# Optimization experiments

Hardware: AMD Instinct MI355X
Metric: run time of the kernel (lower is better)

The kernel has to match this reference:

```python
import jax, jax.numpy as jnp
import numpy as np
import math

MAX_DELAY = 25
TAU = 2.0
VTH = 1.0
BN_EPS = 1e-5
ATAN_ALPHA = 2.0


def build_dcls_kernel(W, P, SIG, D):
    # Gaussian-interpolated DCLS kernel ('gauss' version).
    # W, P, SIG: (O, I, K) -> kernel (O, I, D)
    lim = D // 2
    j = jnp.arange(D, dtype=W.dtype)                      # (D,)
    Pc = jnp.clip(P, -lim, lim) + lim                     # (O, I, K)
    sig = jnp.abs(SIG) + 0.27
    g = jnp.exp(-0.5 * ((j - Pc[..., None]) / sig[..., None]) ** 2)  # (O,I,K,D)
    g = g / (g.sum(-1, keepdims=True) + 1e-7)
    return jnp.einsum('oik,oikd->oid', W, g)


def dcls_conv_positive(x, W, P, SIG, D):
    # Dale-positive: abs(weight) before kernel construction; padding=0 (VALID)
    k = build_dcls_kernel(jnp.abs(W), P, SIG, D)
    return jax.lax.conv_general_dilated(
        x, k, window_strides=(1,), padding='VALID',
        dimension_numbers=('NCW', 'OIW', 'NCW'))


def batchnorm_m(x, gamma, beta):
    # spikingjelly layer.BatchNorm1d step_mode='m' on (T, B, C):
    # flattens (T*B) as batch, normalizes per channel (training-mode stats).
    mean = x.mean(axis=(0, 1))
    var = x.var(axis=(0, 1))
    return (x - mean) * jax.lax.rsqrt(var + BN_EPS) * gamma + beta


def lif_multistep(x_seq, tau, v_th):
    # LIFNode, decay_input=False, v_reset=0 (hard reset), detach_reset=True,
    # ATan surrogate. x_seq: (T, B, C).
    inv_tau = jnp.asarray(1.0 / tau, x_seq.dtype)
    def step(v, xt):
        v = v * (1.0 - inv_tau) + xt              # charge (decay_input=False)
        u = v - v_th
        sg = jnp.arctan(0.5 * math.pi * ATAN_ALPHA * u) / math.pi + 0.5
        hard = (u >= 0).astype(xt.dtype)
        spike = sg + jax.lax.stop_gradient(hard - sg)
        v = v * (1.0 - jax.lax.stop_gradient(spike))   # hard reset, detached
        return v, spike
    v0 = jnp.zeros(x_seq.shape[1:], x_seq.dtype)
    _, spikes = jax.lax.scan(step, v0, x_seq)
    return spikes


def setup_inputs() -> dict:
    key = jax.random.key(0)
    ks = jax.random.split(key, 8)
    B, C_in, T = 64, 700, 300
    n_out, n_inh, K = 256, 128, 1
    return {
        'x': jax.random.normal(ks[0], (B, C_in, T), jnp.float32),
        'W_inh': jax.random.normal(ks[1], (n_inh, C_in, K), jnp.float32),
        'P_inh': jax.random.normal(ks[2], (n_inh, C_in, K), jnp.float32),
        'SIG_inh': jax.random.uniform(ks[3], (n_inh, C_in, K), jnp.float32),
        'W_exc': jax.random.normal(ks[4], (n_out, C_in, K), jnp.float32),
        'P_exc': jax.random.normal(ks[5], (n_out, C_in, K), jnp.float32),
        'SIG_exc': jax.random.uniform(ks[6], (n_out, C_in, K), jnp.float32),
        'w_exc_inh': jax.random.uniform(ks[7], (n_out, n_inh), jnp.float32),
        'bn_gamma': jnp.ones((n_inh,), jnp.float32),
        'bn_beta': jnp.zeros((n_inh,), jnp.float32),
    }


def reference(x, W_inh, P_inh, SIG_inh, W_exc, P_exc, SIG_exc, w_exc_inh,
              bn_gamma, bn_beta):
    # inhibitory branch
    in_inhib = dcls_conv_positive(x, W_inh, P_inh, SIG_inh, MAX_DELAY)  # (B,Ci,T')
    in_inhib = jnp.transpose(in_inhib, (2, 0, 1))                       # (T',B,Ci)
    in_inhib = batchnorm_m(in_inhib, bn_gamma, bn_beta)
    spikes = lif_multistep(in_inhib, TAU, VTH)                          # (T',B,Ci)
    out_inhib = jnp.einsum('tbi,oi->tbo', spikes, -jnp.abs(w_exc_inh))
    out_inhib = jnp.transpose(out_inhib, (1, 2, 0))                     # (B,O,T')
    # excitatory branch
    excit = dcls_conv_positive(x, W_exc, P_exc, SIG_exc, MAX_DELAY)     # (B,O,T')
    return excit + out_inhib
```

## Files before the change

### kernel.cpp

```cpp
#include <hip/hip_runtime.h>
#include <math.h>

#define CI   700
#define TIN  300
#define DD   25
#define TOUT 276
#define BB   64
#define OINH 128
#define OEXC 256

#define TROWS 312
#define IPAD  704

typedef __attribute__((ext_vector_type(8))) short short8;
typedef __attribute__((ext_vector_type(4))) float f32x4;
typedef __attribute__((ext_vector_type(8))) unsigned short ushort8v;

static __device__ __forceinline__ unsigned short f2bf(float f) {
    unsigned int u = __float_as_uint(f);
    unsigned int r = (u + 0x7FFFu + ((u >> 16) & 1u)) >> 16;
    return (unsigned short)r;
}
static __device__ __forceinline__ float bf2f(unsigned short h) {
    return __uint_as_float(((unsigned int)h) << 16);
}

static __device__ __forceinline__ void gload_lds16(const void* g, void* l) {
    __builtin_amdgcn_global_load_lds(
        (const __attribute__((address_space(1))) unsigned int*)g,
        (__attribute__((address_space(3))) unsigned int*)l, 16, 0, 0);
}

__global__ void build_kt(const float* __restrict__ W, const float* __restrict__ P,
                         const float* __restrict__ SIG, float* __restrict__ kt, int O) {
    int n = blockIdx.x * 256 + threadIdx.x;
    if (n >= O * CI) return;
    int o = n % O;
    int i = n / O;
    float w   = fabsf(W[o * CI + i]);
    float p   = fminf(fmaxf(P[o * CI + i], -12.f), 12.f) + 12.f;
    float sig = fabsf(SIG[o * CI + i]) + 0.27f;
    float inv = 1.f / sig;
    float g[DD];
    float sum = 0.f;
#pragma unroll
    for (int d = 0; d < DD; ++d) {
        float e = ((float)d - p) * inv;
        g[d] = expf(-0.5f * e * e);
        sum += g[d];
    }
    float sc = w / (sum + 1e-7f);
#pragma unroll
    for (int d = 0; d < DD; ++d)
        kt[(i * DD + d) * O + o] = g[d] * sc;
}

__global__ void kexc_build(const float* __restrict__ W, const float* __restrict__ P,
                           const float* __restrict__ SIG, unsigned short* __restrict__ kb2) {
    int n = blockIdx.x * 256 + threadIdx.x;
    if (n >= OEXC * IPAD) return;
    int o = n / IPAD, ip = n % IPAD;
    if (ip >= CI) {
#pragma unroll
        for (int d = 0; d < DD; ++d)
            kb2[((size_t)d * OEXC + o) * IPAD + ip] = 0;
        return;
    }
    float w   = fabsf(W[o * CI + ip]);
    float p   = fminf(fmaxf(P[o * CI + ip], -12.f), 12.f) + 12.f;
    float sig = fabsf(SIG[o * CI + ip]) + 0.27f;
    float inv = 1.f / sig;
    float g[DD];
    float sum = 0.f;
#pragma unroll
    for (int d = 0; d < DD; ++d) {
        float e = ((float)d - p) * inv;
        g[d] = expf(-0.5f * e * e);
        sum += g[d];
    }
    float sc = w / (sum + 1e-7f);
#pragma unroll
    for (int d = 0; d < DD; ++d)
        kb2[((size_t)d * OEXC + o) * IPAD + ip] = f2bf(g[d] * sc);
}

__global__ void kinh_build(const float* __restrict__ W, const float* __restrict__ P,
                           const float* __restrict__ SIG,
                           unsigned short* __restrict__ kbh, unsigned short* __restrict__ kbl) {
    int n = blockIdx.x * 256 + threadIdx.x;
    if (n >= OINH * IPAD) return;
    int o = n / IPAD, ip = n % IPAD;
    if (ip >= CI) {
#pragma unroll
        for (int d = 0; d < DD; ++d) {
            kbh[((size_t)d * OINH + o) * IPAD + ip] = 0;
            kbl[((size_t)d * OINH + o) * IPAD + ip] = 0;
        }
        return;
    }
    float w   = fabsf(W[o * CI + ip]);
    float p   = fminf(fmaxf(P[o * CI + ip], -12.f), 12.f) + 12.f;
    float sig = fabsf(SIG[o * CI + ip]) + 0.27f;
    float inv = 1.f / sig;
    float g[DD];
    float sum = 0.f;
#pragma unroll
    for (int d = 0; d < DD; ++d) {
        float e = ((float)d - p) * inv;
        g[d] = expf(-0.5f * e * e);
        sum += g[d];
    }
    float sc = w / (sum + 1e-7f);
#pragma unroll
    for (int d = 0; d < DD; ++d) {
        float v = g[d] * sc;
        unsigned short h = f2bf(v);
        kbh[((size_t)d * OINH + o) * IPAD + ip] = h;
        kbl[((size_t)d * OINH + o) * IPAD + ip] = f2bf(v - bf2f(h));
    }
}

__global__ __launch_bounds__(256)
void xt_kernel(const float* __restrict__ x, unsigned short* __restrict__ xTh,
               unsigned short* __restrict__ xTl) {
    __shared__ float tile[64][65];
    const int tid = threadIdx.x;
    const int t0 = blockIdx.x * 64, i0 = blockIdx.y * 64, b = blockIdx.z;
#pragma unroll
    for (int s = 0; s < 16; ++s) {
        int f = s * 256 + tid;
        int tt = f & 63, ii = f >> 6;
        float v = 0.f;
        if (t0 + tt < TIN && i0 + ii < CI)
            v = x[((size_t)b * CI + i0 + ii) * TIN + t0 + tt];
        tile[tt][ii] = v;
    }
    __syncthreads();
#pragma unroll
    for (int s = 0; s < 2; ++s) {
        int f = s * 256 + tid;
        int tt = f >> 3, g = f & 7;
        if (t0 + tt < TROWS) {
            ushort8v vh, vl;
#pragma unroll
            for (int e = 0; e < 8; ++e) {
                float v = tile[tt][g * 8 + e];
                unsigned short h = f2bf(v);
                vh[e] = h;
                vl[e] = f2bf(v - bf2f(h));
            }
            size_t off = ((size_t)b * TROWS + t0 + tt) * IPAD + i0 + g * 8;
            *(ushort8v*)(xTh + off) = vh;
            if (xTl) *(ushort8v*)(xTl + off) = vl;
        }
    }
}

__global__ void wt_kernel(const float* __restrict__ w, float* __restrict__ wt) {
    int n = blockIdx.x * 256 + threadIdx.x;
    if (n >= OINH * OEXC) return;
    int o = n % OEXC, c = n / OEXC;
    wt[c * OEXC + o] = -fabsf(w[o * OINH + c]);
}

__global__ __launch_bounds__(128)
void conv_fused_v3(const unsigned short* __restrict__ xTh, const unsigned short* __restrict__ xTl,
                   const unsigned short* __restrict__ kb2,
                   const unsigned short* __restrict__ kbh, const unsigned short* __restrict__ kbl,
                   float* __restrict__ pexc0, float* __restrict__ pexc1,
                   float* __restrict__ pinh0, float* __restrict__ pinh1) {
    __shared__ unsigned short lds[20480];

    const int tid  = threadIdx.x;
    const int wave = tid >> 6;
    const int lane = tid & 63;
    const int l15 = lane & 15, l4 = lane >> 4;
    const int tt   = blockIdx.x % 3;
    const int ksp  = blockIdx.x / 3;
    const int role = blockIdx.y;
    const int b    = blockIdx.z;
    const int t0   = tt * 96;
    const int icb  = ksp * 11;

    const int ld_r = lane >> 2;
    const int ld_c = (((lane & 3) ^ ((lane >> 3) & 3)) << 4);
    const int SA   = (l15 >> 1) & 3;

    const size_t xstride = (size_t)IPAD * 2;
    const char* xh_base = (const char*)xTh + ((size_t)b * TROWS + t0) * xstride;
    const char* xl_base = (const char*)xTl + ((size_t)b * TROWS + t0) * xstride;

    if (role < 2) {
        unsigned short* xs = lds;
        unsigned short* ks = lds + 4096;
        const int o0 = role * 128 + wave * 64;

        f32x4 acc[4][6];
#pragma unroll
        for (int i = 0; i < 4; ++i)
#pragma unroll
            for (int j = 0; j < 6; ++j) acc[i][j] = (f32x4)0.f;

        for (int c = 0; c < 11; ++c) {
            const size_t cb = (size_t)(icb + c) * 64;
            __syncthreads();
            for (int j = wave; j < 8; j += 2)
                gload_lds16(xh_base + (size_t)(16 * j + ld_r) * xstride + cb + ld_c,
                            (char*)xs + j * 1024);
#pragma unroll
            for (int q = 0; q < 2; ++q) {
                const char* kbase = (const char*)kb2 + ((size_t)(q * OEXC) + o0) * xstride + cb;
                char* kdst = (char*)ks + (q * 2 + wave) * 4096;
#pragma unroll
                for (int j = 0; j < 4; ++j)
                    gload_lds16(kbase + (size_t)(16 * j + ld_r) * xstride + ld_c,
                                kdst + j * 1024);
            }
            asm volatile("s_waitcnt vmcnt(4)" ::: "memory");
            __syncthreads();

            int cur = 0;
            for (int d = 0; d < DD; ++d) {
                if (d < DD - 2) {
                    int nb = cur + 2; if (nb >= 3) nb -= 3;
                    const char* kbase = (const char*)kb2 +
                        ((size_t)((d + 2) * OEXC) + o0) * xstride + cb;
                    char* kdst = (char*)ks + (nb * 2 + wave) * 4096;
#pragma unroll
                    for (int j = 0; j < 4; ++j)
                        gload_lds16(kbase + (size_t)(16 * j + ld_r) * xstride + ld_c,
                                    kdst + j * 1024);
                }
                const char* kp = (const char*)ks + (cur * 2 + wave) * 4096;
                short8 A[4];
#pragma unroll
                for (int i = 0; i < 4; ++i)
                    A[i] = *(const short8*)(kp + (i * 16 + l15) * 64 + ((l4 ^ SA) << 4));
#pragma unroll
                for (int j = 0; j < 6; ++j) {
                    const int tr = j * 16 + l15 + d;
                    short8 Bv = *(const short8*)((const char*)xs + tr * 64 +
                                                 ((l4 ^ ((tr >> 1) & 3)) << 4));
#pragma unroll
                    for (int i = 0; i < 4; ++i)
                        acc[i][j] = __builtin_amdgcn_mfma_f32_16x16x32_bf16(
                            A[i], Bv, acc[i][j], 0, 0, 0);
                }
                if (d < DD - 2)
                    asm volatile("s_waitcnt vmcnt(4)" ::: "memory");
                else if (d == DD - 2)
                    asm volatile("s_waitcnt vmcnt(0)" ::: "memory");
                cur = (cur == 2) ? 0 : cur + 1;
            }
        }
        float* dst = ksp ? pexc1 : pexc0;
#pragma unroll
        for (int i = 0; i < 4; ++i)
#pragma unroll
            for (int j = 0; j < 6; ++j) {
                const int t = t0 + j * 16 + l15;
                if (t < TOUT) {
                    float* op = dst + ((size_t)b * OEXC + o0 + i * 16 + l4 * 4) * TOUT + t;
#pragma unroll
                    for (int r = 0; r < 4; ++r) op[(size_t)r * TOUT] = acc[i][j][r];
                }
            }
    } else {
        unsigned short* xsh = lds;
        unsigned short* xsl = lds + 4096;
        unsigned short* kws = lds + 8192;
        const int o0  = (role - 2) * 64;
        const int o0w = o0 + wave * 32;

        f32x4 acc[2][6];
#pragma unroll
        for (int i = 0; i < 2; ++i)
#pragma unroll
            for (int j = 0; j < 6; ++j) acc[i][j] = (f32x4)0.f;

        for (int c = 0; c < 11; ++c) {
            const size_t cb = (size_t)(icb + c) * 64;
            __syncthreads();
            for (int j = wave; j < 8; j += 2) {
                gload_lds16(xh_base + (size_t)(16 * j + ld_r) * xstride + cb + ld_c,
                            (char*)xsh + j * 1024);
                gload_lds16(xl_base + (size_t)(16 * j + ld_r) * xstride + cb + ld_c,
                            (char*)xsl + j * 1024);
            }
#pragma unroll
            for (int q = 0; q < 2; ++q) {
                const size_t ko = ((size_t)(q * OINH) + o0w) * xstride + cb;
                char* kdst = (char*)kws + (q * 2 + wave) * 4096;
#pragma unroll
                for (int j = 0; j < 2; ++j) {
                    gload_lds16((const char*)kbh + ko + (size_t)(16 * j + ld_r) * xstride + ld_c,
                                kdst + j * 1024);
                    gload_lds16((const char*)kbl + ko + (size_t)(16 * j + ld_r) * xstride + ld_c,
                                kdst + 2048 + j * 1024);
                }
            }
            asm volatile("s_waitcnt vmcnt(4)" ::: "memory");
            __syncthreads();

            int cur = 0;
            for (int d = 0; d < DD; ++d) {
                if (d < DD - 2) {
                    int nb = cur + 2; if (nb >= 3) nb -= 3;
                    const size_t ko = ((size_t)((d + 2) * OINH) + o0w) * xstride + cb;
                    char* kdst = (char*)kws + (nb * 2 + wave) * 4096;
#pragma unroll
                    for (int j = 0; j < 2; ++j) {
                        gload_lds16((const char*)kbh + ko + (size_t)(16 * j + ld_r) * xstride + ld_c,
                                    kdst + j * 1024);
                        gload_lds16((const char*)kbl + ko + (size_t)(16 * j + ld_r) * xstride + ld_c,
                                    kdst + 2048 + j * 1024);
                    }
                }
                const char* kp = (const char*)kws + (cur * 2 + wave) * 4096;
                short8 Ah[2], Al[2];
#pragma unroll
                for (int i = 0; i < 2; ++i) {
                    Ah[i] = *(const short8*)(kp + (i * 16 + l15) * 64 + ((l4 ^ SA) << 4));
                    Al[i] = *(const short8*)(kp + 2048 + (i * 16 + l15) * 64 + ((l4 ^ SA) << 4));
                }
#pragma unroll
                for (int j = 0; j < 6; ++j) {
                    const int tr = j * 16 + l15 + d;
                    const int xo = tr * 64 + ((l4 ^ ((tr >> 1) & 3)) << 4);
                    short8 Bh = *(const short8*)((const char*)xsh + xo);
                    short8 Bl = *(const short8*)((const char*)xsl + xo);
#pragma unroll
                    for (int i = 0; i < 2; ++i) {
                        acc[i][j] = __builtin_amdgcn_mfma_f32_16x16x32_bf16(
                            Ah[i], Bh, acc[i][j], 0, 0, 0);
                        acc[i][j] = __builtin_amdgcn_mfma_f32_16x16x32_bf16(
                            Ah[i], Bl, acc[i][j], 0, 0, 0);
                        acc[i][j] = __builtin_amdgcn_mfma_f32_16x16x32_bf16(
                            Al[i], Bh, acc[i][j], 0, 0, 0);
                    }
                }
                if (d < DD - 2)
                    asm volatile("s_waitcnt vmcnt(4)" ::: "memory");
                else if (d == DD - 2)
                    asm volatile("s_waitcnt vmcnt(0)" ::: "memory");
                cur = (cur == 2) ? 0 : cur + 1;
            }
        }
        float* dst = ksp ? pinh1 : pinh0;
#pragma unroll
        for (int i = 0; i < 2; ++i)
#pragma unroll
            for (int j = 0; j < 6; ++j) {
                const int t = t0 + j * 16 + l15;
                if (t < TOUT) {
                    float* op = dst + ((size_t)b * OINH + o0w + i * 16 + l4 * 4) * TOUT + t;
#pragma unroll
                    for (int r = 0; r < 4; ++r) op[(size_t)r * TOUT] = acc[i][j][r];
                }
            }
    }
}

__global__ void add_exc(const float* __restrict__ p1, float* __restrict__ out) {
    int n = blockIdx.x * 256 + threadIdx.x;
    float4 a = ((const float4*)out)[n];
    float4 v = ((const float4*)p1)[n];
    a.x += v.x; a.y += v.y; a.z += v.z; a.w += v.w;
    ((float4*)out)[n] = a;
}

__global__ void bn_stats2(float* __restrict__ cinh, const float* __restrict__ q1,
                          const float* __restrict__ gamma, const float* __restrict__ beta,
                          float* __restrict__ scale, float* __restrict__ shift) {
    const int c = blockIdx.x, tid = threadIdx.x;
    float sum = 0.f, sq = 0.f;
    for (int idx = tid; idx < BB * TOUT; idx += 256) {
        int b = idx / TOUT, t = idx - b * TOUT;
        size_t off = (size_t)(b * OINH + c) * TOUT + t;
        float v = cinh[off] + q1[off];
        cinh[off] = v;
        sum += v; sq += v * v;
    }
#pragma unroll
    for (int off = 32; off; off >>= 1) {
        sum += __shfl_down(sum, off);
        sq  += __shfl_down(sq, off);
    }
    __shared__ float ls[8];
    int wid = tid >> 6;
    if ((tid & 63) == 0) { ls[wid * 2] = sum; ls[wid * 2 + 1] = sq; }
    __syncthreads();
    if (tid == 0) {
        float S = 0.f, Q = 0.f;
#pragma unroll
        for (int wv = 0; wv < 4; ++wv) { S += ls[wv * 2]; Q += ls[wv * 2 + 1]; }
        const float n = (float)(BB * TOUT);
        float mean = S / n;
        float var  = Q / n - mean * mean;
        float rs   = 1.f / sqrtf(var + 1e-5f);
        float sc   = gamma[c] * rs;
        scale[c] = sc;
        shift[c] = beta[c] - mean * sc;
    }
}

__global__ __launch_bounds__(128)
void lif2(const float* __restrict__ cinh, const float* __restrict__ scale,
          const float* __restrict__ shift, unsigned char* __restrict__ spk) {
    __shared__ float tile[128 * 65];
    const int b = blockIdx.x, c = threadIdx.x;
    const float sc = scale[c], sh = shift[c];
    const float* base = cinh + (size_t)b * OINH * TOUT;
    float v = 0.f;
    for (int tc = 0; tc < TOUT; tc += 64) {
        const int len = (TOUT - tc < 64) ? (TOUT - tc) : 64;
        const int L4 = len >> 2;
        __syncthreads();
        for (int q = c; q < 128 * L4; q += 128) {
            int cc = q / L4, e = q - cc * L4;
            float4 vv = *(const float4*)(base + (size_t)cc * TOUT + tc + e * 4);
            float* dstp = &tile[cc * 65 + e * 4];
            dstp[0] = vv.x; dstp[1] = vv.y; dstp[2] = vv.z; dstp[3] = vv.w;
        }
        __syncthreads();
        for (int t2 = 0; t2 < len; ++t2) {
            float xin = tile[c * 65 + t2] * sc + sh;
            v = 0.5f * v + xin;
            bool s = (v >= 1.f);
            spk[((size_t)(tc + t2) * BB + b) * OINH + c] = s ? 1 : 0;
            v = s ? 0.f : v;
        }
    }
}

__global__ __launch_bounds__(128)
void conv_mfma(const unsigned short* __restrict__ xTh, const unsigned short* __restrict__ kb2,
               float* __restrict__ out) {
    __shared__ unsigned short xs[120 * 64];
    __shared__ unsigned short ks[2][2][64 * 64];

    const int tid  = threadIdx.x;
    const int wave = tid >> 6;
    const int lane = tid & 63;
    const int l15 = lane & 15, l4 = lane >> 4, l7 = lane & 7;
    const int b  = blockIdx.z;
    const int t0 = blockIdx.x * 96;
    const int o0 = blockIdx.y * 128 + wave * 64;

    const int ld_row = lane >> 3;
    const int ld_swz = ((l7 ^ ld_row) << 4);

    f32x4 acc[4][6];
#pragma unroll
    for (int i = 0; i < 4; ++i)
#pragma unroll
        for (int j = 0; j < 6; ++j) acc[i][j] = (f32x4)0.f;

    const char* xrow0 = (const char*)xTh + ((size_t)b * TROWS + t0) * (IPAD * 2);

    for (int ic = 0; ic < 11; ++ic) {
        const int ic0 = ic * 64;
        __syncthreads();
        for (int j = wave; j < 15; j += 2)
            gload_lds16(xrow0 + (size_t)(8 * j + ld_row) * (IPAD * 2) + ic0 * 2 + ld_swz,
                        (char*)xs + j * 1024);
        {
            const char* ksrc = (const char*)kb2 + ((size_t)o0) * (IPAD * 2) + ic0 * 2;
            char* kdst = (char*)ks + (0 * 2 + wave) * 8192;
#pragma unroll
            for (int j = 0; j < 8; ++j)
                gload_lds16(ksrc + (size_t)(8 * j + ld_row) * (IPAD * 2) + ld_swz,
                            kdst + j * 1024);
        }
        asm volatile("s_waitcnt vmcnt(0)" ::: "memory");
        __syncthreads();

        for (int d = 0; d < DD; ++d) {
            const int cur = d & 1;
            if (d < DD - 1) {
                const char* ksrc = (const char*)kb2 +
                    ((size_t)(d + 1) * OEXC + o0) * (IPAD * 2) + ic0 * 2;
                char* kdst = (char*)ks + ((cur ^ 1) * 2 + wave) * 8192;
#pragma unroll
                for (int j = 0; j < 8; ++j)
                    gload_lds16(ksrc + (size_t)(8 * j + ld_row) * (IPAD * 2) + ld_swz,
                                kdst + j * 1024);
            }
            const char* kp = (const char*)ks + (cur * 2 + wave) * 8192;
#pragma unroll
            for (int ks2 = 0; ks2 < 2; ++ks2) {
                const int cg = ks2 * 4 + l4;
                short8 A[4];
#pragma unroll
                for (int i = 0; i < 4; ++i)
                    A[i] = *(const short8*)(kp + (i * 16 + l15) * 128 + ((cg ^ l7) << 4));
#pragma unroll
                for (int j = 0; j < 6; ++j) {
                    const int tr = j * 16 + l15 + d;
                    short8 Bv = *(const short8*)((const char*)xs + tr * 128 +
                                                 ((cg ^ (tr & 7)) << 4));
#pragma unroll
                    for (int i = 0; i < 4; ++i)
                        acc[i][j] = __builtin_amdgcn_mfma_f32_16x16x32_bf16(
                            A[i], Bv, acc[i][j], 0, 0, 0);
                }
            }
            asm volatile("s_waitcnt vmcnt(0)" ::: "memory");
        }
    }

#pragma unroll
    for (int i = 0; i < 4; ++i)
#pragma unroll
        for (int j = 0; j < 6; ++j) {
            const int tt = t0 + j * 16 + l15;
            if (tt < TOUT) {
                float* op = out + ((size_t)b * OEXC + o0 + i * 16 + l4 * 4) * TOUT + tt;
#pragma unroll
                for (int r = 0; r < 4; ++r) op[(size_t)r * TOUT] = acc[i][j][r];
            }
        }
}

__global__ __launch_bounds__(128)
void conv_mfma_inh(const unsigned short* __restrict__ xTh, const unsigned short* __restrict__ xTl,
                   const unsigned short* __restrict__ kbh, const unsigned short* __restrict__ kbl,
                   float* __restrict__ cinh) {
    __shared__ unsigned short xsh[120 * 64];
    __shared__ unsigned short xsl[120 * 64];
    __shared__ unsigned short ksh[2][64 * 64];
    __shared__ unsigned short ksl[2][64 * 64];

    const int tid  = threadIdx.x;
    const int wave = tid >> 6;
    const int lane = tid & 63;
    const int l15 = lane & 15, l4 = lane >> 4, l7 = lane & 7;
    const int b  = blockIdx.z;
    const int t0 = blockIdx.x * 96;
    const int o0 = blockIdx.y * 64;
    const int wtb = wave * 48;

    const int ld_row = lane >> 3;
    const int ld_swz = ((l7 ^ ld_row) << 4);

    f32x4 acc[4][3];
#pragma unroll
    for (int i = 0; i < 4; ++i)
#pragma unroll
        for (int j = 0; j < 3; ++j) acc[i][j] = (f32x4)0.f;

    const char* xrh = (const char*)xTh + ((size_t)b * TROWS + t0) * (IPAD * 2);
    const char* xrl = (const char*)xTl + ((size_t)b * TROWS + t0) * (IPAD * 2);
    const unsigned short* kb = wave ? kbl : kbh;

    for (int ic = 0; ic < 11; ++ic) {
        const int ic0 = ic * 64;
        __syncthreads();
        for (int j = wave; j < 15; j += 2) {
            gload_lds16(xrh + (size_t)(8 * j + ld_row) * (IPAD * 2) + ic0 * 2 + ld_swz,
                        (char*)xsh + j * 1024);
            gload_lds16(xrl + (size_t)(8 * j + ld_row) * (IPAD * 2) + ic0 * 2 + ld_swz,
                        (char*)xsl + j * 1024);
        }
        {
            char* kd = wave ? (char*)ksl[0] : (char*)ksh[0];
#pragma unroll
            for (int j = 0; j < 8; ++j)
                gload_lds16((const char*)kb +
                                ((size_t)(0 * OINH + o0 + 8 * j + ld_row)) * (IPAD * 2) +
                                ic0 * 2 + ld_swz,
                            kd + j * 1024);
        }
        asm volatile("s_waitcnt vmcnt(0)" ::: "memory");
        __syncthreads();

        for (int d = 0; d < DD; ++d) {
            const int cur = d & 1;
            if (d < DD - 1) {
                char* kd = wave ? (char*)ksl[cur ^ 1] : (char*)ksh[cur ^ 1];
#pragma unroll
                for (int j = 0; j < 8; ++j)
                    gload_lds16((const char*)kb +
                                    ((size_t)((d + 1) * OINH + o0 + 8 * j + ld_row)) * (IPAD * 2) +
                                    ic0 * 2 + ld_swz,
                                kd + j * 1024);
            }
            const char* kph = (const char*)ksh[cur];
            const char* kpl = (const char*)ksl[cur];
#pragma unroll
            for (int k2 = 0; k2 < 2; ++k2) {
                const int cg = k2 * 4 + l4;
                short8 Ah[4], Al[4];
#pragma unroll
                for (int i = 0; i < 4; ++i) {
                    Ah[i] = *(const short8*)(kph + (i * 16 + l15) * 128 + ((cg ^ l7) << 4));
                    Al[i] = *(const short8*)(kpl + (i * 16 + l15) * 128 + ((cg ^ l7) << 4));
                }
#pragma unroll
                for (int j = 0; j < 3; ++j) {
                    const int tr = wtb + j * 16 + l15 + d;
                    short8 Bh = *(const short8*)((const char*)xsh + tr * 128 +
                                                 ((cg ^ (tr & 7)) << 4));
                    short8 Bl = *(const short8*)((const char*)xsl + tr * 128 +
                                                 ((cg ^ (tr & 7)) << 4));
#pragma unroll
                    for (int i = 0; i < 4; ++i) {
                        acc[i][j] = __builtin_amdgcn_mfma_f32_16x16x32_bf16(
                            Ah[i], Bh, acc[i][j], 0, 0, 0);
                        acc[i][j] = __builtin_amdgcn_mfma_f32_16x16x32_bf16(
                            Ah[i], Bl, acc[i][j], 0, 0, 0);
                        acc[i][j] = __builtin_amdgcn_mfma_f32_16x16x32_bf16(
                            Al[i], Bh, acc[i][j], 0, 0, 0);
                    }
                }
            }
            asm volatile("s_waitcnt vmcnt(0)" ::: "memory");
            __syncthreads();
        }
    }

#pragma unroll
    for (int i = 0; i < 4; ++i)
#pragma unroll
        for (int j = 0; j < 3; ++j) {
            const int tt = t0 + wtb + j * 16 + l15;
            if (tt < TOUT) {
                float* op = cinh + ((size_t)b * OINH + o0 + i * 16 + l4 * 4) * TOUT + tt;
#pragma unroll
                for (int r = 0; r < 4; ++r) op[(size_t)r * TOUT] = acc[i][j][r];
            }
        }
}

__global__ void bn_stats(const float* __restrict__ cinh, const float* __restrict__ gamma,
                         const float* __restrict__ beta, float* __restrict__ scale,
                         float* __restrict__ shift) {
    const int c = blockIdx.x, tid = threadIdx.x;
    float sum = 0.f, sq = 0.f;
    for (int idx = tid; idx < BB * TOUT; idx += 256) {
        int b = idx / TOUT, t = idx - b * TOUT;
        float v = cinh[(size_t)(b * OINH + c) * TOUT + t];
        sum += v; sq += v * v;
    }
#pragma unroll
    for (int off = 32; off; off >>= 1) {
        sum += __shfl_down(sum, off);
        sq  += __shfl_down(sq, off);
    }
    __shared__ float ls[8];
    int wid = tid >> 6;
    if ((tid & 63) == 0) { ls[wid * 2] = sum; ls[wid * 2 + 1] = sq; }
    __syncthreads();
    if (tid == 0) {
        float S = 0.f, Q = 0.f;
#pragma unroll
        for (int wv = 0; wv < 4; ++wv) { S += ls[wv * 2]; Q += ls[wv * 2 + 1]; }
        const float n = (float)(BB * TOUT);
        float mean = S / n;
        float var  = Q / n - mean * mean;
        float rs   = 1.f / sqrtf(var + 1e-5f);
        float sc   = gamma[c] * rs;
        scale[c] = sc;
        shift[c] = beta[c] - mean * sc;
    }
}

__global__ __launch_bounds__(256)
void finale(const unsigned char* __restrict__ spk, const float* __restrict__ wt,
            float* __restrict__ out) {
    __shared__ float s_lds[64 * 129];
    const int tid = threadIdx.x;
    const int tx = tid & 15, ty = tid >> 4;
    const int b = blockIdx.z, t0 = blockIdx.x * 64, o0 = blockIdx.y * 64;

#pragma unroll
    for (int s = 0; s < 32; ++s) {
        int f = tid + s * 256;
        int tt = f >> 7, c = f & 127;
        float v = 0.f;
        if (t0 + tt < TOUT) v = (float)spk[((size_t)(t0 + tt) * BB + b) * OINH + c];
        s_lds[tt * 129 + c] = v;
    }
    __syncthreads();

    float acc[4][4] = {{0.f}};
#pragma unroll 4
    for (int c = 0; c < 128; ++c) {
        float4 wv = *(const float4*)(wt + c * OEXC + o0 + ty * 4);
        float wvv[4] = {wv.x, wv.y, wv.z, wv.w};
        float sv[4];
#pragma unroll
        for (int rt = 0; rt < 4; ++rt) sv[rt] = s_lds[(tx * 4 + rt) * 129 + c];
#pragma unroll
        for (int ro = 0; ro < 4; ++ro)
#pragma unroll
            for (int rt = 0; rt < 4; ++rt)
                acc[ro][rt] += wvv[ro] * sv[rt];
    }

    const int tvalid = TOUT - t0;
    if (tx * 4 < tvalid) {
#pragma unroll
        for (int ro = 0; ro < 4; ++ro) {
            float* op = out + (size_t)(b * OEXC + o0 + ty * 4 + ro) * TOUT + t0 + tx * 4;
            float4 v = *(float4*)op;
            v.x += acc[ro][0]; v.y += acc[ro][1]; v.z += acc[ro][2]; v.w += acc[ro][3];
            *(float4*)op = v;
        }
    }
}

__global__ void lif_kernel(const float* __restrict__ cinh, const float* __restrict__ scale,
                           const float* __restrict__ shift, unsigned char* __restrict__ spk) {
    const int b = blockIdx.x, c = threadIdx.x;
    const float sc = scale[c], sh = shift[c];
    const float* row = cinh + (size_t)(b * OINH + c) * TOUT;
    float v = 0.f;
    for (int t = 0; t < TOUT; ++t) {
        float xin = row[t] * sc + sh;
        v = 0.5f * v + xin;
        unsigned char s = (v >= 1.f) ? 1 : 0;
        spk[((size_t)t * BB + b) * OINH + c] = s;
        v = (v >= 1.f) ? 0.f : v;
    }
}

extern "C" void kernel_launch(void* const* d_in, const int* in_sizes, int n_in,
                              void* d_out, int out_size, void* d_ws, size_t ws_size,
                              hipStream_t stream) {
    const float* x       = (const float*)d_in[0];
    const float* W_inh   = (const float*)d_in[1];
    const float* P_inh   = (const float*)d_in[2];
    const float* SIG_inh = (const float*)d_in[3];
    const float* W_exc   = (const float*)d_in[4];
    const float* P_exc   = (const float*)d_in[5];
    const float* SIG_exc = (const float*)d_in[6];
    const float* w_ei    = (const float*)d_in[7];
    const float* gamma   = (const float*)d_in[8];
    const float* beta    = (const float*)d_in[9];
    float* out = (float*)d_out;

    const size_t XT_ELEMS   = (size_t)BB * TROWS * IPAD;
    const size_t KEXC_ELEMS = (size_t)DD * OEXC * IPAD;
    const size_t KINH_ELEMS = (size_t)DD * OINH * IPAD;
    const size_t CINH_ELEMS = (size_t)BB * OINH * TOUT;
    const size_t PEXC_ELEMS = (size_t)BB * OEXC * TOUT;

    const size_t NEED_FAST = 2 * XT_ELEMS * 2 + KEXC_ELEMS * 2 + 2 * KINH_ELEMS * 2 +
                             CINH_ELEMS * 4 + OINH * OEXC * 4 + CINH_ELEMS;
    const size_t NEED_FAST2 = (2 * XT_ELEMS + KEXC_ELEMS + 2 * KINH_ELEMS) * 2 +
                              (PEXC_ELEMS + 2 * CINH_ELEMS + OINH * OEXC + 256) * 4 +
                              CINH_ELEMS;

    if (ws_size >= NEED_FAST2) {
        unsigned short* xTh = (unsigned short*)d_ws;
        unsigned short* xTl = xTh + XT_ELEMS;
        unsigned short* kb2 = xTl + XT_ELEMS;
        unsigned short* kbh = kb2 + KEXC_ELEMS;
        unsigned short* kbl = kbh + KINH_ELEMS;
        float* pexc1 = (float*)(kbl + KINH_ELEMS);
        float* cinh  = pexc1 + PEXC_ELEMS;
        float* pinh1 = cinh + CINH_ELEMS;
        float* wt    = pinh1 + CINH_ELEMS;
        float* scale = wt + OINH * OEXC;
        float* shift = scale + OINH;
        unsigned char* spk = (unsigned char*)(shift + OINH);

        hipLaunchKernelGGL(kexc_build, dim3((OEXC * IPAD + 255) / 256), dim3(256), 0, stream,
                           W_exc, P_exc, SIG_exc, kb2);
        hipLaunchKernelGGL(kinh_build, dim3((OINH * IPAD + 255) / 256), dim3(256), 0, stream,
                           W_inh, P_inh, SIG_inh, kbh, kbl);
        hipLaunchKernelGGL(xt_kernel, dim3(5, 11, 64), dim3(256), 0, stream, x, xTh, xTl);
        hipLaunchKernelGGL(wt_kernel, dim3(128), dim3(256), 0, stream, w_ei, wt);

        hipLaunchKernelGGL(conv_fused_v3, dim3(6, 4, 64), dim3(128), 0, stream,
                           xTh, xTl, kb2, kbh, kbl, out, pexc1, cinh, pinh1);

        hipLaunchKernelGGL(add_exc, dim3((unsigned)(PEXC_ELEMS / 4 / 256)), dim3(256), 0, stream,
                           pexc1, out);
        hipLaunchKernelGGL(bn_stats2, dim3(128), dim3(256), 0, stream,
                           cinh, pinh1, gamma, beta, scale, shift);
        hipLaunchKernelGGL(lif2, dim3(64), dim3(128), 0, stream, cinh, scale, shift, spk);
        hipLaunchKernelGGL(finale, dim3(5, 4, 64), dim3(256), 0, stream, spk, wt, out);
    } else if (ws_size >= NEED_FAST) {
        unsigned short* xTh = (unsigned short*)d_ws;
        unsigned short* xTl = xTh + XT_ELEMS;
        unsigned short* kb2 = xTl + XT_ELEMS;
        unsigned short* kbh = kb2 + KEXC_ELEMS;
        unsigned short* kbl = kbh + KINH_ELEMS;
        float* cinh  = (float*)(kbl + KINH_ELEMS);
        float* wt    = cinh + CINH_ELEMS;
        float* scale = wt + OINH * OEXC;
        float* shift = scale + OINH;
        unsigned char* spk = (unsigned char*)(shift + OINH);

        hipLaunchKernelGGL(kexc_build, dim3((OEXC * IPAD + 255) / 256), dim3(256), 0, stream,
                           W_exc, P_exc, SIG_exc, kb2);
        hipLaunchKernelGGL(kinh_build, dim3((OINH * IPAD + 255) / 256), dim3(256), 0, stream,
                           W_inh, P_inh, SIG_inh, kbh, kbl);
        hipLaunchKernelGGL(xt_kernel, dim3(5, 11, 64), dim3(256), 0, stream, x, xTh, xTl);
        hipLaunchKernelGGL(wt_kernel, dim3(128), dim3(256), 0, stream, w_ei, wt);

        hipLaunchKernelGGL(conv_mfma, dim3(3, 2, 64), dim3(128), 0, stream, xTh, kb2, out);
        hipLaunchKernelGGL(conv_mfma_inh, dim3(3, 2, 64), dim3(128), 0, stream,
                           xTh, xTl, kbh, kbl, cinh);

        hipLaunchKernelGGL(bn_stats, dim3(128), dim3(256), 0, stream, cinh, gamma, beta, scale, shift);
        hipLaunchKernelGGL(lif_kernel, dim3(64), dim3(128), 0, stream, cinh, scale, shift, spk);
        hipLaunchKernelGGL(finale, dim3(5, 4, 64), dim3(256), 0, stream, spk, wt, out);
    } else {
        unsigned short* xTh = (unsigned short*)d_ws;
        unsigned short* kb2 = xTh + XT_ELEMS;
        float* kt_inh = (float*)(kb2 + KEXC_ELEMS);
        float* cinh   = kt_inh + 2240000;
        float* wt     = cinh + CINH_ELEMS;
        float* scale  = wt + OINH * OEXC;
        float* shift  = scale + OINH;
        unsigned char* spk = (unsigned char*)(shift + OINH);

        hipLaunchKernelGGL(kexc_build, dim3((OEXC * IPAD + 255) / 256), dim3(256), 0, stream,
                           W_exc, P_exc, SIG_exc, kb2);
        hipLaunchKernelGGL(build_kt, dim3(350), dim3(256), 0, stream,
                           W_inh, P_inh, SIG_inh, kt_inh, OINH);
        hipLaunchKernelGGL(xt_kernel, dim3(5, 11, 64), dim3(256), 0, stream, x, xTh,
                           (unsigned short*)nullptr);
        hipLaunchKernelGGL(wt_kernel, dim3(128), dim3(256), 0, stream, w_ei, wt);

        hipLaunchKernelGGL(conv_mfma, dim3(3, 2, 64), dim3(128), 0, stream, xTh, kb2, out);
        extern __global__ void conv_dcls_fb(const float*, const float*, float*, int);
        hipLaunchKernelGGL(conv_dcls_fb, dim3(5, 1, 64), dim3(256), 0, stream, x, kt_inh, cinh, OINH);

        hipLaunchKernelGGL(bn_stats, dim3(128), dim3(256), 0, stream, cinh, gamma, beta, scale, shift);
        hipLaunchKernelGGL(lif_kernel, dim3(64), dim3(128), 0, stream, cinh, scale, shift, spk);
        hipLaunchKernelGGL(finale, dim3(5, 4, 64), dim3(256), 0, stream, spk, wt, out);
    }
}

__global__ __launch_bounds__(256)
void conv_dcls_fb(const float* __restrict__ x, const float* __restrict__ kt,
                  float* __restrict__ out, int O) {
    __shared__ float k_lds[100 * 128];
    __shared__ float x_lds[4 * 88];

    const int tid = threadIdx.x;
    const int tx = tid & 7;
    const int ty = tid >> 3;
    const int b  = blockIdx.z;
    const int t0 = blockIdx.x * 64;
    const int o0 = blockIdx.y * 128;
    const int tlim = TIN - t0;

    float acc[4][8];
#pragma unroll
    for (int ro = 0; ro < 4; ++ro)
#pragma unroll
        for (int rt = 0; rt < 8; ++rt) acc[ro][rt] = 0.f;

    for (int chunk = 0; chunk < 175; ++chunk) {
        const int i0 = chunk * 4;
        __syncthreads();
#pragma unroll
        for (int s = 0; s < 13; ++s) {
            int f = tid + s * 256;
            if (f < 3200) {
                int j = f >> 5, o4 = f & 31;
                ((float4*)k_lds)[f] =
                    *(const float4*)(kt + (size_t)(i0 * DD + j) * O + o0 + o4 * 4);
            }
        }
        if (tid < 88) {
            int icc = tid / 22, wq = tid % 22;
            float4 v = make_float4(0.f, 0.f, 0.f, 0.f);
            if (wq * 4 < tlim)
                v = *(const float4*)(x + (size_t)(b * CI + i0 + icc) * TIN + t0 + wq * 4);
            ((float4*)x_lds)[tid] = v;
        }
        __syncthreads();
#pragma unroll
        for (int icc = 0; icc < 4; ++icc) {
            float xv[32];
#pragma unroll
            for (int wq = 0; wq < 8; ++wq)
                *(float4*)(xv + 4 * wq) = ((const float4*)(x_lds + icc * 88))[tx * 2 + wq];
#pragma unroll
            for (int d = 0; d < DD; ++d) {
                float4 kv = ((const float4*)(k_lds + (icc * DD + d) * 128))[ty];
                float kvv[4] = {kv.x, kv.y, kv.z, kv.w};
#pragma unroll
                for (int ro = 0; ro < 4; ++ro)
#pragma unroll
                    for (int rt = 0; rt < 8; ++rt)
                        acc[ro][rt] += kvv[ro] * xv[rt + d];
            }
        }
    }
    const int tvalid = TOUT - t0;
#pragma unroll
    for (int ro = 0; ro < 4; ++ro) {
        float* op = out + (size_t)(b * O + o0 + ty * 4 + ro) * TOUT + t0;
#pragma unroll
        for (int u = 0; u < 2; ++u) {
            int toff = tx * 8 + u * 4;
            if (toff < tvalid) {
                float4 v = make_float4(acc[ro][u * 4 + 0], acc[ro][u * 4 + 1],
                                       acc[ro][u * 4 + 2], acc[ro][u * 4 + 3]);
                *(float4*)(op + toff) = v;
            }
        }
    }
}
```

Before: 566.2 us.

## Load conv kernel weights directly to registers and double-buffer x tiles in LDS

The fused conv kernel no longer stages DCLS weight tiles through a triple-buffered LDS ring. Each wave now reads its MFMA A-operands straight from global memory into registers, prefetching the next delay's weights one step ahead. The x tile moves to a double buffer, so the next channel chunk loads while the current one is computed. This cuts LDS usage and per-chunk barriers, but it relies on cache hits for weight reads, which are strided by IPAD, and puts global-load latency on the MFMA critical path. Some kernel definitions are also moved around the file.

```diff
diff --git a/kernel.cpp b/kernel.cpp
--- a/kernel.cpp
+++ b/kernel.cpp
@@ -164,12 +164,12 @@
 }
 
 __global__ __launch_bounds__(128)
-void conv_fused_v3(const unsigned short* __restrict__ xTh, const unsigned short* __restrict__ xTl,
+void conv_fused_v4(const unsigned short* __restrict__ xTh, const unsigned short* __restrict__ xTl,
                    const unsigned short* __restrict__ kb2,
                    const unsigned short* __restrict__ kbh, const unsigned short* __restrict__ kbl,
                    float* __restrict__ pexc0, float* __restrict__ pexc1,
                    float* __restrict__ pinh0, float* __restrict__ pinh1) {
-    __shared__ unsigned short lds[20480];
+    __shared__ unsigned short lds[16384];
 
     const int tid  = threadIdx.x;
     const int wave = tid >> 6;
@@ -184,15 +184,14 @@
 
     const int ld_r = lane >> 2;
     const int ld_c = (((lane & 3) ^ ((lane >> 3) & 3)) << 4);
-    const int SA   = (l15 >> 1) & 3;
 
     const size_t xstride = (size_t)IPAD * 2;
     const char* xh_base = (const char*)xTh + ((size_t)b * TROWS + t0) * xstride;
     const char* xl_base = (const char*)xTl + ((size_t)b * TROWS + t0) * xstride;
 
     if (role < 2) {
-        unsigned short* xs = lds;
-        unsigned short* ks = lds + 4096;
+        unsigned short* xs0 = lds;
+        unsigned short* xs1 = lds + 4096;
         const int o0 = role * 128 + wave * 64;
 
         f32x4 acc[4][6];
@@ -201,57 +200,53 @@
 #pragma unroll
             for (int j = 0; j < 6; ++j) acc[i][j] = (f32x4)0.f;
 
-        for (int c = 0; c < 11; ++c) {
-            const size_t cb = (size_t)(icb + c) * 64;
-            __syncthreads();
+        {
+            const size_t cb = (size_t)icb * 64;
             for (int j = wave; j < 8; j += 2)
                 gload_lds16(xh_base + (size_t)(16 * j + ld_r) * xstride + cb + ld_c,
-                            (char*)xs + j * 1024);
-#pragma unroll
-            for (int q = 0; q < 2; ++q) {
-                const char* kbase = (const char*)kb2 + ((size_t)(q * OEXC) + o0) * xstride + cb;
-                char* kdst = (char*)ks + (q * 2 + wave) * 4096;
-#pragma unroll
-                for (int j = 0; j < 4; ++j)
-                    gload_lds16(kbase + (size_t)(16 * j + ld_r) * xstride + ld_c,
-                                kdst + j * 1024);
-            }
-            asm volatile("s_waitcnt vmcnt(4)" ::: "memory");
-            __syncthreads();
-
-            int cur = 0;
+                            (char*)xs0 + j * 1024);
+        }
+        asm volatile("s_waitcnt vmcnt(0)" ::: "memory");
+        __syncthreads();
+
+        for (int c = 0; c < 11; ++c) {
+            unsigned short* xc = (c & 1) ? xs1 : xs0;
+            unsigned short* xn = (c & 1) ? xs0 : xs1;
+            if (c < 10) {
+                const size_t cbn = (size_t)(icb + c + 1) * 64;
+                for (int j = wave; j < 8; j += 2)
+                    gload_lds16(xh_base + (size_t)(16 * j + ld_r) * xstride + cbn + ld_c,
+                                (char*)xn + j * 1024);
+            }
+            const size_t che = (size_t)(icb + c) * 32 + l4 * 8;
+            short8 Ac[4], An[4];
+#pragma unroll
+            for (int i = 0; i < 4; ++i)
+                Ac[i] = *(const short8*)(kb2 + ((size_t)(o0 + i * 16 + l15)) * IPAD + che);
             for (int d = 0; d < DD; ++d) {
-                if (d < DD - 2) {
-                    int nb = cur + 2; if (nb >= 3) nb -= 3;
-                    const char* kbase = (const char*)kb2 +
-                        ((size_t)((d + 2) * OEXC) + o0) * xstride + cb;
-                    char* kdst = (char*)ks + (nb * 2 + wave) * 4096;
-#pragma unroll
-                    for (int j = 0; j < 4; ++j)
-                        gload_lds16(kbase + (size_t)(16 * j + ld_r) * xstride + ld_c,
-                                    kdst + j * 1024);
-                }
-                const char* kp = (const char*)ks + (cur * 2 + wave) * 4096;
-                short8 A[4];
-#pragma unroll
-                for (int i = 0; i < 4; ++i)
-                    A[i] = *(const short8*)(kp + (i * 16 + l15) * 64 + ((l4 ^ SA) << 4));
+                if (d < DD - 1) {
+#pragma unroll
+                    for (int i = 0; i < 4; ++i)
+                        An[i] = *(const short8*)(kb2 +
+                            ((size_t)((d + 1) * OEXC) + o0 + i * 16 + l15) * IPAD + che);
+                }
 #pragma unroll
                 for (int j = 0; j < 6; ++j) {
                     const int tr = j * 16 + l15 + d;
-                    short8 Bv = *(const short8*)((const char*)xs + tr * 64 +
+                    short8 Bv = *(const short8*)((const char*)xc + tr * 64 +
                                                  ((l4 ^ ((tr >> 1) & 3)) << 4));
 #pragma unroll
                     for (int i = 0; i < 4; ++i)
                         acc[i][j] = __builtin_amdgcn_mfma_f32_16x16x32_bf16(
-                            A[i], Bv, acc[i][j], 0, 0, 0);
-                }
-                if (d < DD - 2)
-                    asm volatile("s_waitcnt vmcnt(4)" ::: "memory");
-                else if (d == DD - 2)
-                    asm volatile("s_waitcnt vmcnt(0)" ::: "memory");
-                cur = (cur == 2) ? 0 : cur + 1;
-            }
+                            Ac[i], Bv, acc[i][j], 0, 0, 0);
+                }
+                if (d < DD - 1) {
+#pragma unroll
+                    for (int i = 0; i < 4; ++i) Ac[i] = An[i];
+                }
+            }
+            asm volatile("s_waitcnt vmcnt(0)" ::: "memory");
+            __syncthreads();
         }
         float* dst = ksp ? pexc1 : pexc0;
 #pragma unroll
@@ -266,11 +261,11 @@
                 }
             }
     } else {
-        unsigned short* xsh = lds;
-        unsigned short* xsl = lds + 4096;
-        unsigned short* kws = lds + 8192;
-        const int o0  = (role - 2) * 64;
-        const int o0w = o0 + wave * 32;
+        unsigned short* xh0 = lds;
+        unsigned short* xh1 = lds + 4096;
+        unsigned short* xl0 = lds + 8192;
+        unsigned short* xl1 = lds + 12288;
+        const int o0w = (role - 2) * 64 + wave * 32;
 
         f32x4 acc[2][6];
 #pragma unroll
@@ -278,73 +273,72 @@
 #pragma unroll
             for (int j = 0; j < 6; ++j) acc[i][j] = (f32x4)0.f;
 
-        for (int c = 0; c < 11; ++c) {
-            const size_t cb = (size_t)(icb + c) * 64;
-            __syncthreads();
+        {
+            const size_t cb = (size_t)icb * 64;
             for (int j = wave; j < 8; j += 2) {
                 gload_lds16(xh_base + (size_t)(16 * j + ld_r) * xstride + cb + ld_c,
-                            (char*)xsh + j * 1024);
+                            (char*)xh0 + j * 1024);
                 gload_lds16(xl_base + (size_t)(16 * j + ld_r) * xstride + cb + ld_c,
-                            (char*)xsl + j * 1024);
-            }
-#pragma unroll
-            for (int q = 0; q < 2; ++q) {
-                const size_t ko = ((size_t)(q * OINH) + o0w) * xstride + cb;
-                char* kdst = (char*)kws + (q * 2 + wave) * 4096;
-#pragma unroll
-                for (int j = 0; j < 2; ++j) {
-                    gload_lds16((const char*)kbh + ko + (size_t)(16 * j + ld_r) * xstride + ld_c,
-                                kdst + j * 1024);
-                    gload_lds16((const char*)kbl + ko + (size_t)(16 * j + ld_r) * xstride + ld_c,
-                                kdst + 2048 + j * 1024);
-                }
-            }
-            asm volatile("s_waitcnt vmcnt(4)" ::: "memory");
-            __syncthreads();
-
-            int cur = 0;
+                            (char*)xl0 + j * 1024);
+            }
+        }
+        asm volatile("s_waitcnt vmcnt(0)" ::: "memory");
+        __syncthreads();
+
+        for (int c = 0; c < 11; ++c) {
+            unsigned short* xch = (c & 1) ? xh1 : xh0;
+            unsigned short* xnh = (c & 1) ? xh0 : xh1;
+            unsigned short* xcl = (c & 1) ? xl1 : xl0;
+            unsigned short* xnl = (c & 1) ? xl0 : xl1;
+            if (c < 10) {
+                const size_t cbn = (size_t)(icb + c + 1) * 64;
+                for (int j = wave; j < 8; j += 2) {
+                    gload_lds16(xh_base + (size_t)(16 * j + ld_r) * xstride + cbn + ld_c,
+                                (char*)xnh + j * 1024);
+                    gload_lds16(xl_base + (size_t)(16 * j + ld_r) * xstride + cbn + ld_c,
+                                (char*)xnl + j * 1024);
+                }
+            }
+            const size_t che = (size_t)(icb + c) * 32 + l4 * 8;
+            short8 Ahc[2], Alc[2], Ahn[2], Aln[2];
+#pragma unroll
+            for (int i = 0; i < 2; ++i) {
+                const size_t ro = ((size_t)(o0w + i * 16 + l15)) * IPAD + che;
+                Ahc[i] = *(const short8*)(kbh + ro);
+                Alc[i] = *(const short8*)(kbl + ro);
+            }
             for (int d = 0; d < DD; ++d) {
-                if (d < DD - 2) {
-                    int nb = cur + 2; if (nb >= 3) nb -= 3;
-                    const size_t ko = ((size_t)((d + 2) * OINH) + o0w) * xstride + cb;
-                    char* kdst = (char*)kws + (nb * 2 + wave) * 4096;
-#pragma unroll
-                    for (int j = 0; j < 2; ++j) {
-                        gload_lds16((const char*)kbh + ko + (size_t)(16 * j + ld_r) * xstride + ld_c,
-                                    kdst + j * 1024);
-                        gload_lds16((const char*)kbl + ko + (size_t)(16 * j + ld_r) * xstride + ld_c,
-                                    kdst + 2048 + j * 1024);
+                if (d < DD - 1) {
+#pragma unroll
+                    for (int i = 0; i < 2; ++i) {
+                        const size_t ro = ((size_t)((d + 1) * OINH) + o0w + i * 16 + l15) * IPAD + che;
+                        Ahn[i] = *(const short8*)(kbh + ro);
+                        Aln[i] = *(const short8*)(kbl + ro);
                     }
-                }
-                const char* kp = (const char*)kws + (cur * 2 + wave) * 4096;
-                short8 Ah[2], Al[2];
-#pragma unroll
-                for (int i = 0; i < 2; ++i) {
-                    Ah[i] = *(const short8*)(kp + (i * 16 + l15) * 64 + ((l4 ^ SA) << 4));
-                    Al[i] = *(const short8*)(kp + 2048 + (i * 16 + l15) * 64 + ((l4 ^ SA) << 4));
                 }
 #pragma unroll
                 for (int j = 0; j < 6; ++j) {
                     const int tr = j * 16 + l15 + d;
                     const int xo = tr * 64 + ((l4 ^ ((tr >> 1) & 3)) << 4);
-                    short8 Bh = *(const short8*)((const char*)xsh + xo);
-                    short8 Bl = *(const short8*)((const char*)xsl + xo);
+                    short8 Bh = *(const short8*)((const char*)xch + xo);
+                    short8 Bl = *(const short8*)((const char*)xcl + xo);
 #pragma unroll
                     for (int i = 0; i < 2; ++i) {
                         acc[i][j] = __builtin_amdgcn_mfma_f32_16x16x32_bf16(
-                            Ah[i], Bh, acc[i][j], 0, 0, 0);
+                            Ahc[i], Bh, acc[i][j], 0, 0, 0);
                         acc[i][j] = __builtin_amdgcn_mfma_f32_16x16x32_bf16(
-                            Ah[i], Bl, acc[i][j], 0, 0, 0);
+                            Ahc[i], Bl, acc[i][j], 0, 0, 0);
                         acc[i][j] = __builtin_amdgcn_mfma_f32_16x16x32_bf16(
-                            Al[i], Bh, acc[i][j], 0, 0, 0);
+                            Alc[i], Bh, acc[i][j], 0, 0, 0);
                     }
                 }
-                if (d < DD - 2)
-                    asm volatile("s_waitcnt vmcnt(4)" ::: "memory");
-                else if (d == DD - 2)
-                    asm volatile("s_waitcnt vmcnt(0)" ::: "memory");
-                cur = (cur == 2) ? 0 : cur + 1;
-            }
+                if (d < DD - 1) {
+#pragma unroll
+                    for (int i = 0; i < 2; ++i) { Ahc[i] = Ahn[i]; Alc[i] = Aln[i]; }
+                }
+            }
+            asm volatile("s_waitcnt vmcnt(0)" ::: "memory");
+            __syncthreads();
         }
         float* dst = ksp ? pinh1 : pinh0;
 #pragma unroll
@@ -632,6 +626,80 @@
         }
 }
 
+__global__ __launch_bounds__(256)
+void conv_dcls_fb(const float* __restrict__ x, const float* __restrict__ kt,
+                  float* __restrict__ out, int O) {
+    __shared__ float k_lds[100 * 128];
+    __shared__ float x_lds[4 * 88];
+
+    const int tid = threadIdx.x;
+    const int tx = tid & 7;
+    const int ty = tid >> 3;
+    const int b  = blockIdx.z;
+    const int t0 = blockIdx.x * 64;
+    const int o0 = blockIdx.y * 128;
+    const int tlim = TIN - t0;
+
+    float acc[4][8];
+#pragma unroll
+    for (int ro = 0; ro < 4; ++ro)
+#pragma unroll
+        for (int rt = 0; rt < 8; ++rt) acc[ro][rt] = 0.f;
+
+    for (int chunk = 0; chunk < 175; ++chunk) {
+        const int i0 = chunk * 4;
+        __syncthreads();
+#pragma unroll
+        for (int s = 0; s < 13; ++s) {
+            int f = tid + s * 256;
+            if (f < 3200) {
+                int j = f >> 5, o4 = f & 31;
+                ((float4*)k_lds)[f] =
+                    *(const float4*)(kt + (size_t)(i0 * DD + j) * O + o0 + o4 * 4);
+            }
+        }
+        if (tid < 88) {
+            int icc = tid / 22, wq = tid % 22;
+            float4 v = make_float4(0.f, 0.f, 0.f, 0.f);
+            if (wq * 4 < tlim)
+                v = *(const float4*)(x + (size_t)(b * CI + i0 + icc) * TIN + t0 + wq * 4);
+            ((float4*)x_lds)[tid] = v;
+        }
+        __syncthreads();
+#pragma unroll
+        for (int icc = 0; icc < 4; ++icc) {
+            float xv[32];
+#pragma unroll
+            for (int wq = 0; wq < 8; ++wq)
+                *(float4*)(xv + 4 * wq) = ((const float4*)(x_lds + icc * 88))[tx * 2 + wq];
+#pragma unroll
+            for (int d = 0; d < DD; ++d) {
+                float4 kv = ((const float4*)(k_lds + (icc * DD + d) * 128))[ty];
+                float kvv[4] = {kv.x, kv.y, kv.z, kv.w};
+#pragma unroll
+                for (int ro = 0; ro < 4; ++ro)
+#pragma unroll
+                    for (int rt = 0; rt < 8; ++rt)
+                        acc[ro][rt] += kvv[ro] * xv[rt + d];
+            }
+        }
+    }
+    const int tvalid = TOUT - t0;
+#pragma unroll
+    for (int ro = 0; ro < 4; ++ro) {
+        float* op = out + (size_t)(b * O + o0 + ty * 4 + ro) * TOUT + t0;
+#pragma unroll
+        for (int u = 0; u < 2; ++u) {
+            int toff = tx * 8 + u * 4;
+            if (toff < tvalid) {
+                float4 v = make_float4(acc[ro][u * 4 + 0], acc[ro][u * 4 + 1],
+                                       acc[ro][u * 4 + 2], acc[ro][u * 4 + 3]);
+                *(float4*)(op + toff) = v;
+            }
+        }
+    }
+}
+
 __global__ void bn_stats(const float* __restrict__ cinh, const float* __restrict__ gamma,
                          const float* __restrict__ beta, float* __restrict__ scale,
                          float* __restrict__ shift) {
@@ -662,51 +730,6 @@
         float sc   = gamma[c] * rs;
         scale[c] = sc;
         shift[c] = beta[c] - mean * sc;
-    }
-}
-
-__global__ __launch_bounds__(256)
-void finale(const unsigned char* __restrict__ spk, const float* __restrict__ wt,
-            float* __restrict__ out) {
-    __shared__ float s_lds[64 * 129];
-    const int tid = threadIdx.x;
-    const int tx = tid & 15, ty = tid >> 4;
-    const int b = blockIdx.z, t0 = blockIdx.x * 64, o0 = blockIdx.y * 64;
-
-#pragma unroll
-    for (int s = 0; s < 32; ++s) {
-        int f = tid + s * 256;
-        int tt = f >> 7, c = f & 127;
-        float v = 0.f;
-        if (t0 + tt < TOUT) v = (float)spk[((size_t)(t0 + tt) * BB + b) * OINH + c];
-        s_lds[tt * 129 + c] = v;
-    }
-    __syncthreads();
-
-    float acc[4][4] = {{0.f}};
-#pragma unroll 4
-    for (int c = 0; c < 128; ++c) {
-        float4 wv = *(const float4*)(wt + c * OEXC + o0 + ty * 4);
-        float wvv[4] = {wv.x, wv.y, wv.z, wv.w};
-        float sv[4];
-#pragma unroll
-        for (int rt = 0; rt < 4; ++rt) sv[rt] = s_lds[(tx * 4 + rt) * 129 + c];
-#pragma unroll
-        for (int ro = 0; ro < 4; ++ro)
-#pragma unroll
-            for (int rt = 0; rt < 4; ++rt)
-                acc[ro][rt] += wvv[ro] * sv[rt];
-    }
-
-    const int tvalid = TOUT - t0;
-    if (tx * 4 < tvalid) {
-#pragma unroll
-        for (int ro = 0; ro < 4; ++ro) {
-            float* op = out + (size_t)(b * OEXC + o0 + ty * 4 + ro) * TOUT + t0 + tx * 4;
-            float4 v = *(float4*)op;
-            v.x += acc[ro][0]; v.y += acc[ro][1]; v.z += acc[ro][2]; v.w += acc[ro][3];
-            *(float4*)op = v;
-        }
     }
 }
 
@@ -722,6 +745,51 @@
         unsigned char s = (v >= 1.f) ? 1 : 0;
         spk[((size_t)t * BB + b) * OINH + c] = s;
         v = (v >= 1.f) ? 0.f : v;
+    }
+}
+
+__global__ __launch_bounds__(256)
+void finale(const unsigned char* __restrict__ spk, const float* __restrict__ wt,
+            float* __restrict__ out) {
+    __shared__ float s_lds[64 * 129];
+    const int tid = threadIdx.x;
+    const int tx = tid & 15, ty = tid >> 4;
+    const int b = blockIdx.z, t0 = blockIdx.x * 64, o0 = blockIdx.y * 64;
+
+#pragma unroll
+    for (int s = 0; s < 32; ++s) {
+        int f = tid + s * 256;
+        int tt = f >> 7, c = f & 127;
+        float v = 0.f;
+        if (t0 + tt < TOUT) v = (float)spk[((size_t)(t0 + tt) * BB + b) * OINH + c];
+        s_lds[tt * 129 + c] = v;
+    }
+    __syncthreads();
+
+    float acc[4][4] = {{0.f}};
+#pragma unroll 4
+    for (int c = 0; c < 128; ++c) {
+        float4 wv = *(const float4*)(wt + c * OEXC + o0 + ty * 4);
+        float wvv[4] = {wv.x, wv.y, wv.z, wv.w};
+        float sv[4];
+#pragma unroll
+        for (int rt = 0; rt < 4; ++rt) sv[rt] = s_lds[(tx * 4 + rt) * 129 + c];
+#pragma unroll
+        for (int ro = 0; ro < 4; ++ro)
+#pragma unroll
+            for (int rt = 0; rt < 4; ++rt)
+                acc[ro][rt] += wvv[ro] * sv[rt];
+    }
+
+    const int tvalid = TOUT - t0;
+    if (tx * 4 < tvalid) {
+#pragma unroll
+        for (int ro = 0; ro < 4; ++ro) {
+            float* op = out + (size_t)(b * OEXC + o0 + ty * 4 + ro) * TOUT + t0 + tx * 4;
+            float4 v = *(float4*)op;
+            v.x += acc[ro][0]; v.y += acc[ro][1]; v.z += acc[ro][2]; v.w += acc[ro][3];
+            *(float4*)op = v;
+        }
     }
 }
 
@@ -773,7 +841,7 @@
         hipLaunchKernelGGL(xt_kernel, dim3(5, 11, 64), dim3(256), 0, stream, x, xTh, xTl);
         hipLaunchKernelGGL(wt_kernel, dim3(128), dim3(256), 0, stream, w_ei, wt);
 
-        hipLaunchKernelGGL(conv_fused_v3, dim3(6, 4, 64), dim3(128), 0, stream,
+        hipLaunchKernelGGL(conv_fused_v4, dim3(6, 4, 64), dim3(128), 0, stream,
                            xTh, xTl, kb2, kbh, kbl, out, pexc1, cinh, pinh1);
 
         hipLaunchKernelGGL(add_exc, dim3((unsigned)(PEXC_ELEMS / 4 / 256)), dim3(256), 0, stream,
@@ -827,7 +895,6 @@
         hipLaunchKernelGGL(wt_kernel, dim3(128), dim3(256), 0, stream, w_ei, wt);
 
         hipLaunchKernelGGL(conv_mfma, dim3(3, 2, 64), dim3(128), 0, stream, xTh, kb2, out);
-        extern __global__ void conv_dcls_fb(const float*, const float*, float*, int);
         hipLaunchKernelGGL(conv_dcls_fb, dim3(5, 1, 64), dim3(256), 0, stream, x, kt_inh, cinh, OINH);
 
         hipLaunchKernelGGL(bn_stats, dim3(128), dim3(256), 0, stream, cinh, gamma, beta, scale, shift);
@@ -835,77 +902,3 @@
         hipLaunchKernelGGL(finale, dim3(5, 4, 64), dim3(256), 0, stream, spk, wt, out);
     }
 }
-
-__global__ __launch_bounds__(256)
-void conv_dcls_fb(const float* __restrict__ x, const float* __restrict__ kt,
-                  float* __restrict__ out, int O) {
-    __shared__ float k_lds[100 * 128];
-    __shared__ float x_lds[4 * 88];
-
-    const int tid = threadIdx.x;
-    const int tx = tid & 7;
-    const int ty = tid >> 3;
-    const int b  = blockIdx.z;
-    const int t0 = blockIdx.x * 64;
-    const int o0 = blockIdx.y * 128;
-    const int tlim = TIN - t0;
-
-    float acc[4][8];
-#pragma unroll
-    for (int ro = 0; ro < 4; ++ro)
-#pragma unroll
-        for (int rt = 0; rt < 8; ++rt) acc[ro][rt] = 0.f;
-
-    for (int chunk = 0; chunk < 175; ++chunk) {
-        const int i0 = chunk * 4;
-        __syncthreads();
-#pragma unroll
-        for (int s = 0; s < 13; ++s) {
-            int f = tid + s * 256;
-            if (f < 3200) {
-                int j = f >> 5, o4 = f & 31;
-                ((float4*)k_lds)[f] =
-                    *(const float4*)(kt + (size_t)(i0 * DD + j) * O + o0 + o4 * 4);
-            }
-        }
-        if (tid < 88) {
-            int icc = tid / 22, wq = tid % 22;
-            float4 v = make_float4(0.f, 0.f, 0.f, 0.f);
-            if (wq * 4 < tlim)
-                v = *(const float4*)(x + (size_t)(b * CI + i0 + icc) * TIN + t0 + wq * 4);
-            ((float4*)x_lds)[tid] = v;
-        }
-        __syncthreads();
-#pragma unroll
-        for (int icc = 0; icc < 4; ++icc) {
-            float xv[32];
-#pragma unroll
-            for (int wq = 0; wq < 8; ++wq)
-                *(float4*)(xv + 4 * wq) = ((const float4*)(x_lds + icc * 88))[tx * 2 + wq];
-#pragma unroll
-            for (int d = 0; d < DD; ++d) {
-                float4 kv = ((const float4*)(k_lds + (icc * DD + d) * 128))[ty];
-                float kvv[4] = {kv.x, kv.y, kv.z, kv.w};
-#pragma unroll
-                for (int ro = 0; ro < 4; ++ro)
-#pragma unroll
-                    for (int rt = 0; rt < 8; ++rt)
-                        acc[ro][rt] += kvv[ro] * xv[rt + d];
-            }
-        }
-    }
-    const int tvalid = TOUT - t0;
-#pragma unroll
-    for (int ro = 0; ro < 4; ++ro) {
-        float* op = out + (size_t)(b * O + o0 + ty * 4 + ro) * TOUT + t0;
-#pragma unroll
-        for (int u = 0; u < 2; ++u) {
-            int toff = tx * 8 + u * 4;
-            if (toff < tvalid) {
-                float4 v = make_float4(acc[ro][u * 4 + 0], acc[ro][u * 4 + 1],
-                                       acc[ro][u * 4 + 2], acc[ro][u * 4 + 3]);
-                *(float4*)(op + toff) = v;
-            }
-        }
-    }
-}
```

Result: slower. 607.4 us (+7.3%).
